# Kernel optimization log

Hardware: AMD Instinct MI355X
Metric: run time of the kernel (lower is better)

The kernel has to match this reference:

```python
import jax, jax.numpy as jnp
import numpy as np

B, T, C = 256, 1024, 128


def setup_inputs() -> dict:
    key = jax.random.key(0)
    k1, k2 = jax.random.split(key)
    potentials = jax.random.normal(k1, (B, T, C), dtype=jnp.float32)
    # glorot_uniform init for the [C, C] transition matrix
    limit = float(np.sqrt(6.0 / (C + C)))
    transitions = jax.random.uniform(k2, (C, C), minval=-limit, maxval=limit, dtype=jnp.float32)
    return {"potentials": potentials, "transitions": transitions}


def _viterbi_decode(potentials, transitions):
    """Equivalent of tfa.text.crf.crf_decode with full sequence lengths ('reg' mode).

    potentials: [B, T, C] unary scores; transitions: [C, C] (prev -> cur).
    Returns one-hot decoded tags [B, T, C] (the layer's inference output).
    """
    num_tags = potentials.shape[-1]
    pots_t = jnp.swapaxes(potentials, 0, 1)  # [T, B, C]
    alpha0 = pots_t[0]                        # [B, C]

    def fwd_step(alpha, pot):
        # max-plus DP step: scores[b, p, c] = alpha[b, p] + transitions[p, c]
        scores = alpha[:, :, None] + transitions[None, :, :]   # [B, C, C]
        bp = jnp.argmax(scores, axis=1).astype(jnp.int32)      # backpointers [B, C]
        alpha_new = jnp.max(scores, axis=1) + pot               # [B, C]
        return alpha_new, bp

    alpha_T, bps = jax.lax.scan(fwd_step, alpha0, pots_t[1:])   # bps: [T-1, B, C]
    last_tag = jnp.argmax(alpha_T, axis=-1).astype(jnp.int32)   # [B]

    def bwd_step(tag, bp):
        # tag at time t+1 -> best tag at time t via backpointers
        prev = jnp.take_along_axis(bp, tag[:, None], axis=1)[:, 0]
        return prev, prev

    _, prev_tags = jax.lax.scan(bwd_step, last_tag, bps, reverse=True)  # [T-1, B]
    tags = jnp.concatenate([prev_tags, last_tag[None, :]], axis=0)      # [T, B]
    tags = jnp.swapaxes(tags, 0, 1)                                      # [B, T]
    return jax.nn.one_hot(tags, num_tags, dtype=potentials.dtype)


def reference(potentials, transitions):
    return _viterbi_decode(potentials, transitions)
```

## Files before the change

### kernel.cpp

```cpp
#include <hip/hip_runtime.h>


typedef float f32x2 __attribute__((ext_vector_type(2)));
typedef unsigned int u32x4 __attribute__((ext_vector_type(4)));

constexpr int NB = 256;
constexpr int NT = 1024;
constexpr int NC = 128;

template <int CTRL>
__device__ __forceinline__ float fmax_dpp(float v) {
  int x = __builtin_amdgcn_update_dpp(__float_as_int(v), __float_as_int(v),
                                      CTRL, 0xF, 0xF, false);
  return fmaxf(v, __int_as_float(x));
}
__device__ __forceinline__ float wave_max_to_lane63(float m) {
  m = fmax_dpp<0x111>(m);
  m = fmax_dpp<0x112>(m);
  m = fmax_dpp<0x114>(m);
  m = fmax_dpp<0x118>(m);
  m = fmax_dpp<0x142>(m);
  m = fmax_dpp<0x143>(m);
  return m;
}

constexpr int ABUF = 192;

#define T_C(T0, T1, T2, T3, MD)                              \
  "v_pk_add_f32 v[52:53], v[60:61], %[" T0 "]\n\t"           \
  "v_pk_add_f32 v[54:55], v[62:63], %[" T1 "]\n\t"           \
  "v_pk_add_f32 v[46:47], v[56:57], %[" T2 "]\n\t"           \
  "v_pk_add_f32 v[44:45], v[58:59], %[" T3 "]\n\t"           \
  "v_max3_f32 v52, v52, v53, v54\n\t"                        \
  "v_max3_f32 v55, v55, v46, v47\n\t"                        \
  "v_max3_f32 v52, v52, v55, v44\n\t"                        \
  "v_max_f32 " MD ", v52, v45\n\t"

#define DPP4(CTL)                                                          \
  "v_max_f32_dpp v48, v48, v48 " CTL " row_mask:0xf bank_mask:0xf\n\t"     \
  "v_max_f32_dpp v49, v49, v49 " CTL " row_mask:0xf bank_mask:0xf\n\t"     \
  "v_max_f32_dpp v50, v50, v50 " CTL " row_mask:0xf bank_mask:0xf\n\t"     \
  "v_max_f32_dpp v51, v51, v51 " CTL " row_mask:0xf bank_mask:0xf\n\t"

#define STEP_S(RD, WR, PC, SOFF)                                           \
  "ds_read_b128 v[60:63], %[" RD "]\n\t"                                   \
  "ds_read_b128 v[56:59], %[" RD "] offset:16\n\t"                         \
  "s_waitcnt lgkmcnt(0)\n\t"                                               \
  T_C("t00", "t01", "t02", "t03", "v48")                                   \
  T_C("t10", "t11", "t12", "t13", "v49")                                   \
  T_C("t20", "t21", "t22", "t23", "v50")                                   \
  T_C("t30", "t31", "t32", "t33", "v51")                                   \
  DPP4("quad_perm:[1,0,3,2]")                                              \
  DPP4("quad_perm:[2,3,0,1]")                                              \
  DPP4("row_ror:4")                                                        \
  DPP4("row_ror:8")                                                        \
  "v_cndmask_b32 v46, v48, v49, %[sel1]\n\t"                               \
  "v_cndmask_b32 v47, v50, v51, %[sel1]\n\t"                               \
  "v_cndmask_b32 v47, v46, v47, %[sel2]\n\t"                               \
  "s_mov_b64 exec, %[wmask]\n\t"                                           \
  "v_add_f32 v46, v47, %[" PC "]\n\t"                                      \
  "ds_write_b32 %[" WR "], v46\n\t"                                        \
  "global_store_dword %[qoff], v47, %[sout] offset:" SOFF "\n\t"           \
  "s_mov_b64 exec, -1\n\t"                                                 \
  "s_waitcnt lgkmcnt(0)\n\t"                                               \
  "s_barrier\n\t"

__global__ __launch_bounds__(512, 2)
void crf_fwd(const float* __restrict__ pot, const float* __restrict__ trans,
             float* __restrict__ out) {
  __shared__ __align__(16) float alpha[2 * ABUF];

  const int tid = threadIdx.x;
  const int b = blockIdx.x;
  const int w = tid >> 6;
  const int l = tid & 63;
  const int r = l >> 4;
  const int i = l & 15;
  const int g = w * 4 + r;
  const bool wr = (i >= 12);
  const int cw = 4 * g + (i & 3);
  const int widx = 12 * (cw >> 3) + (cw & 7);

  const float* potb = pot + (size_t)b * NT * NC;
  float* outb = out + (size_t)b * NT * NC;

  const float* tb = trans + (8 * i) * NC + 4 * g;
  float4 L0 = *(const float4*)(tb + 0 * NC);
  float4 L1 = *(const float4*)(tb + 1 * NC);
  float4 L2 = *(const float4*)(tb + 2 * NC);
  float4 L3 = *(const float4*)(tb + 3 * NC);
  float4 L4 = *(const float4*)(tb + 4 * NC);
  float4 L5 = *(const float4*)(tb + 5 * NC);
  float4 L6 = *(const float4*)(tb + 6 * NC);
  float4 L7 = *(const float4*)(tb + 7 * NC);
  f32x2 t00 = {L0.x, L1.x}, t01 = {L2.x, L3.x}, t02 = {L4.x, L5.x}, t03 = {L6.x, L7.x};
  f32x2 t10 = {L0.y, L1.y}, t11 = {L2.y, L3.y}, t12 = {L4.y, L5.y}, t13 = {L6.y, L7.y};
  f32x2 t20 = {L0.z, L1.z}, t21 = {L2.z, L3.z}, t22 = {L4.z, L5.z}, t23 = {L6.z, L7.z};
  f32x2 t30 = {L0.w, L1.w}, t31 = {L2.w, L3.w}, t32 = {L4.w, L5.w}, t33 = {L6.w, L7.w};

  unsigned rda = (unsigned)(size_t)(alpha + 12 * i);
  unsigned rdb = (unsigned)(size_t)(alpha + ABUF + 12 * i);
  unsigned wra = (unsigned)(size_t)(alpha + widx);
  unsigned wrb = (unsigned)(size_t)(alpha + ABUF + widx);

  unsigned qoff = (unsigned)((1 * NC + cw) * 4);
  unsigned poff = ((unsigned)b * (NT * NC) + 5 * NC + cw) * 4u;
  unsigned long long sout = (unsigned long long)(size_t)outb;
  unsigned long long pbase = (unsigned long long)(size_t)pot;
  u32x4 srd;
  srd.x = (unsigned)pbase;
  srd.y = (unsigned)(pbase >> 32) & 0xFFFFu;
  srd.z = (unsigned)(NB * NT * NC) * 4u;
  srd.w = 0x00020000u;
  unsigned long long sel1 = 0xAAAAAAAAAAAAAAAAull;
  unsigned long long sel2 = 0xCCCCCCCCCCCCCCCCull;
  unsigned long long wmask = 0xF000F000F000F000ull;
  int cnt = 254;

  float pc0 = potb[1 * NC + cw], pc1 = potb[2 * NC + cw];
  float pc2 = potb[3 * NC + cw], pc3 = potb[4 * NC + cw];
  float pn0 = 0.f, pn1 = 0.f, pn2 = 0.f, pn3 = 0.f;

  if (wr) {
    alpha[widx] = potb[cw];
    outb[cw] = 0.0f;
  }
  __syncthreads();

  asm volatile(
      "buffer_load_dword %[pn0], %[poff], %[srd], 0 offen\n\t"
      "buffer_load_dword %[pn1], %[poff], %[srd], 0 offen offset:512\n\t"
      "buffer_load_dword %[pn2], %[poff], %[srd], 0 offen offset:1024\n\t"
      "buffer_load_dword %[pn3], %[poff], %[srd], 0 offen offset:1536\n\t"
      "L_crfmain_%=:\n\t"
      STEP_S("rda", "wrb", "pc0", "0")
      STEP_S("rdb", "wra", "pc1", "512")
      STEP_S("rda", "wrb", "pc2", "1024")
      STEP_S("rdb", "wra", "pc3", "1536")
      "s_waitcnt vmcnt(4)\n\t"
      "v_mov_b32 %[pc0], %[pn0]\n\t"
      "v_mov_b32 %[pc1], %[pn1]\n\t"
      "v_mov_b32 %[pc2], %[pn2]\n\t"
      "v_mov_b32 %[pc3], %[pn3]\n\t"
      "v_add_u32 %[poff], 0x800, %[poff]\n\t"
      "v_add_u32 %[qoff], 0x800, %[qoff]\n\t"
      "buffer_load_dword %[pn0], %[poff], %[srd], 0 offen\n\t"
      "buffer_load_dword %[pn1], %[poff], %[srd], 0 offen offset:512\n\t"
      "buffer_load_dword %[pn2], %[poff], %[srd], 0 offen offset:1024\n\t"
      "buffer_load_dword %[pn3], %[poff], %[srd], 0 offen offset:1536\n\t"
      "s_sub_u32 %[cnt], %[cnt], 1\n\t"
      "s_cmp_lg_u32 %[cnt], 0\n\t"
      "s_cbranch_scc1 L_crfmain_%=\n\t"
      STEP_S("rda", "wrb", "pc0", "0")
      STEP_S("rdb", "wra", "pc1", "512")
      STEP_S("rda", "wrb", "pc2", "1024")
      STEP_S("rdb", "wra", "pc3", "1536")
      "s_waitcnt vmcnt(4)\n\t"
      "v_mov_b32 %[pc0], %[pn0]\n\t"
      "v_mov_b32 %[pc1], %[pn1]\n\t"
      "v_mov_b32 %[pc2], %[pn2]\n\t"
      "v_add_u32 %[qoff], 0x800, %[qoff]\n\t"
      STEP_S("rda", "wrb", "pc0", "0")
      STEP_S("rdb", "wra", "pc1", "512")
      STEP_S("rda", "wrb", "pc2", "1024")
      : [pc0] "+v"(pc0), [pc1] "+v"(pc1), [pc2] "+v"(pc2), [pc3] "+v"(pc3),
        [pn0] "+v"(pn0), [pn1] "+v"(pn1), [pn2] "+v"(pn2), [pn3] "+v"(pn3),
        [qoff] "+v"(qoff), [poff] "+v"(poff), [cnt] "+s"(cnt)
      : [t00] "v"(t00), [t01] "v"(t01), [t02] "v"(t02), [t03] "v"(t03),
        [t10] "v"(t10), [t11] "v"(t11), [t12] "v"(t12), [t13] "v"(t13),
        [t20] "v"(t20), [t21] "v"(t21), [t22] "v"(t22), [t23] "v"(t23),
        [t30] "v"(t30), [t31] "v"(t31), [t32] "v"(t32), [t33] "v"(t33),
        [rda] "v"(rda), [rdb] "v"(rdb), [wra] "v"(wra), [wrb] "v"(wrb),
        [sout] "s"(sout), [srd] "s"(srd),
        [sel1] "s"(sel1), [sel2] "s"(sel2), [wmask] "s"(wmask)
      : "memory", "scc",
        "v44", "v45", "v46", "v47", "v48", "v49", "v50", "v51",
        "v52", "v53", "v54", "v55", "v56", "v57", "v58", "v59",
        "v60", "v61", "v62", "v63");
}


__global__ __launch_bounds__(256)
void crf_bwd(const float* __restrict__ pot, const float* __restrict__ trans,
             float* __restrict__ out) {
  extern __shared__ float tTf[];
  const int tid = threadIdx.x;
  const int b = blockIdx.x;
  const float* potb = pot + (size_t)b * NT * NC;
  float* outb = out + (size_t)b * NT * NC;

  {
    const int rr = tid >> 1;
    const int h = tid & 1;
    const float4* src = (const float4*)(trans + rr * NC + h * 64);
    const int lo = rr & 63, hb = rr >> 6;
    #pragma unroll
    for (int j = 0; j < 16; ++j) {
      float4 q = src[j];
      int cb = h * 64 + 4 * j;
      tTf[(cb + 0) * 128 + lo * 2 + hb] = q.x;
      tTf[(cb + 1) * 128 + lo * 2 + hb] = q.y;
      tTf[(cb + 2) * 128 + lo * 2 + hb] = q.z;
      tTf[(cb + 3) * 128 + lo * 2 + hb] = q.w;
    }
  }
  __syncthreads();
  if (tid >= 64) return;
  const int l = tid;
  const f32x2* tTp = (const f32x2*)tTf;

  float qlo_t = outb[(NT - 1) * NC + l];
  float qhi_t = outb[(NT - 1) * NC + 64 + l];
  float alo_t = qlo_t + potb[(NT - 1) * NC + l];
  float ahi_t = qhi_t + potb[(NT - 1) * NC + 64 + l];
  float m0 = wave_max_to_lane63(fmaxf(alo_t, ahi_t));
  float M0 = __int_as_float(__builtin_amdgcn_readlane(__float_as_int(m0), 63));
  unsigned long long bl = __ballot(alo_t == M0);
  unsigned long long bh = __ballot(ahi_t == M0);
  int tag = bl ? (__ffsll((long long)bl) - 1)
               : (64 + __ffsll((long long)bh) - 1);

  float cqlo[8], cqhi[8], calo[8], cahi[8];
  float nqlo[8], nqhi[8], nplo[8], nphi[8];
  #pragma unroll
  for (int j = 0; j < 8; ++j) {
    int rw = NT - 2 - j;
    cqlo[j] = outb[rw * NC + l];
    cqhi[j] = outb[rw * NC + 64 + l];
    calo[j] = cqlo[j] + potb[rw * NC + l];
    cahi[j] = cqhi[j] + potb[rw * NC + 64 + l];
  }

  for (int g = 0; g < 128; ++g) {
    #pragma unroll
    for (int j = 0; j < 8; ++j) {
      int rw = NT - 10 - 8 * g - j;
      if (rw < 0) rw = 0;
      nqlo[j] = outb[rw * NC + l];
      nqhi[j] = outb[rw * NC + 64 + l];
      nplo[j] = potb[rw * NC + l];
      nphi[j] = potb[rw * NC + 64 + l];
    }
    #pragma unroll
    for (int j = 0; j < 8; ++j) {
      int t = NT - 1 - 8 * g - j;
      if (t >= 1) {
        outb[t * NC + l]      = (l == tag) ? 1.0f : 0.0f;
        outb[t * NC + 64 + l] = (64 + l == tag) ? 1.0f : 0.0f;
        int Mlo = __builtin_amdgcn_readlane(__float_as_int(qlo_t), tag & 63);
        int Mhi = __builtin_amdgcn_readlane(__float_as_int(qhi_t), tag & 63);
        float M = __int_as_float((tag < 64) ? Mlo : Mhi);
        f32x2 tt = tTp[tag * 64 + l];
        float vlo = calo[j] + tt.x;
        float vhi = cahi[j] + tt.y;
        unsigned long long el = __ballot(vlo == M);
        unsigned long long eh = __ballot(vhi == M);
        tag = el ? (__ffsll((long long)el) - 1)
                 : (64 + __ffsll((long long)eh) - 1);
        qlo_t = cqlo[j];
        qhi_t = cqhi[j];
      }
    }
    #pragma unroll
    for (int j = 0; j < 8; ++j) {
      cqlo[j] = nqlo[j]; cqhi[j] = nqhi[j];
      calo[j] = nqlo[j] + nplo[j];
      cahi[j] = nqhi[j] + nphi[j];
    }
  }
  outb[l]      = (l == tag) ? 1.0f : 0.0f;
  outb[64 + l] = (64 + l == tag) ? 1.0f : 0.0f;
}


extern "C" void kernel_launch(void* const* d_in, const int* in_sizes, int n_in,
                              void* d_out, int out_size, void* d_ws, size_t ws_size,
                              hipStream_t stream) {
  const float* pot   = (const float*)d_in[0];
  const float* trans = (const float*)d_in[1];
  float* out = (float*)d_out;

  hipFuncSetAttribute((const void*)crf_bwd,
                      hipFuncAttributeMaxDynamicSharedMemorySize, NC * NC * 4);

  crf_fwd<<<NB, 512, 0, stream>>>(pot, trans, out);
  crf_bwd<<<NB, 256, NC * NC * 4, stream>>>(pot, trans, out);
}
```

Baseline: 436.3 us.

## Fuse forward and backward Viterbi kernels with 256-thread blocks, 8 tags per group

Merges the forward max-plus scan and the backtrace into one kernel, removing the second launch. It also halves the forward block to 256 threads, with each group handling 8 tags instead of 4. The transition slice per lane now lives in 64 explicitly named VGPRs, loaded by inline global loads. This doubles per-lane ALU work per step but halves the number of waves that meet at each barrier, and it drops occupancy to one block per CU.

```diff
diff --git a/kernel.cpp b/kernel.cpp
--- a/kernel.cpp
+++ b/kernel.cpp
@@ -26,49 +26,74 @@
 
 constexpr int ABUF = 192;
 
-#define T_C(T0, T1, T2, T3, MD)                              \
-  "v_pk_add_f32 v[52:53], v[60:61], %[" T0 "]\n\t"           \
-  "v_pk_add_f32 v[54:55], v[62:63], %[" T1 "]\n\t"           \
-  "v_pk_add_f32 v[46:47], v[56:57], %[" T2 "]\n\t"           \
-  "v_pk_add_f32 v[44:45], v[58:59], %[" T3 "]\n\t"           \
-  "v_max3_f32 v52, v52, v53, v54\n\t"                        \
-  "v_max3_f32 v55, v55, v46, v47\n\t"                        \
-  "v_max3_f32 v52, v52, v55, v44\n\t"                        \
-  "v_max_f32 " MD ", v52, v45\n\t"
-
-#define DPP4(CTL)                                                          \
+
+#define LDT(R, O) "global_load_dword v" R ", %[toff], %[strans] offset:" O "\n\t"
+
+#define TREE2(A0, A2, A4, A6, MDA, B0, B2, B4, B6, MDB)     \
+  "v_pk_add_f32 v[32:33], v[56:57], v[" A0 "]\n\t"          \
+  "v_pk_add_f32 v[40:41], v[56:57], v[" B0 "]\n\t"          \
+  "v_pk_add_f32 v[34:35], v[58:59], v[" A2 "]\n\t"          \
+  "v_pk_add_f32 v[42:43], v[58:59], v[" B2 "]\n\t"          \
+  "v_pk_add_f32 v[36:37], v[60:61], v[" A4 "]\n\t"          \
+  "v_pk_add_f32 v[44:45], v[60:61], v[" B4 "]\n\t"          \
+  "v_pk_add_f32 v[38:39], v[62:63], v[" A6 "]\n\t"          \
+  "v_pk_add_f32 v[46:47], v[62:63], v[" B6 "]\n\t"          \
+  "v_max3_f32 v32, v32, v33, v34\n\t"                       \
+  "v_max3_f32 v40, v40, v41, v42\n\t"                       \
+  "v_max3_f32 v35, v35, v36, v37\n\t"                       \
+  "v_max3_f32 v43, v43, v44, v45\n\t"                       \
+  "v_max3_f32 v32, v32, v35, v38\n\t"                       \
+  "v_max3_f32 v40, v40, v43, v46\n\t"                       \
+  "v_max_f32 " MDA ", v32, v39\n\t"                         \
+  "v_max_f32 " MDB ", v40, v47\n\t"
+
+#define DPP8(CTL)                                                          \
   "v_max_f32_dpp v48, v48, v48 " CTL " row_mask:0xf bank_mask:0xf\n\t"     \
   "v_max_f32_dpp v49, v49, v49 " CTL " row_mask:0xf bank_mask:0xf\n\t"     \
   "v_max_f32_dpp v50, v50, v50 " CTL " row_mask:0xf bank_mask:0xf\n\t"     \
-  "v_max_f32_dpp v51, v51, v51 " CTL " row_mask:0xf bank_mask:0xf\n\t"
+  "v_max_f32_dpp v51, v51, v51 " CTL " row_mask:0xf bank_mask:0xf\n\t"     \
+  "v_max_f32_dpp v52, v52, v52 " CTL " row_mask:0xf bank_mask:0xf\n\t"     \
+  "v_max_f32_dpp v53, v53, v53 " CTL " row_mask:0xf bank_mask:0xf\n\t"     \
+  "v_max_f32_dpp v54, v54, v54 " CTL " row_mask:0xf bank_mask:0xf\n\t"     \
+  "v_max_f32_dpp v55, v55, v55 " CTL " row_mask:0xf bank_mask:0xf\n\t"
 
 #define STEP_S(RD, WR, PC, SOFF)                                           \
-  "ds_read_b128 v[60:63], %[" RD "]\n\t"                                   \
-  "ds_read_b128 v[56:59], %[" RD "] offset:16\n\t"                         \
+  "ds_read_b128 v[56:59], %[" RD "]\n\t"                                   \
+  "ds_read_b128 v[60:63], %[" RD "] offset:16\n\t"                         \
   "s_waitcnt lgkmcnt(0)\n\t"                                               \
-  T_C("t00", "t01", "t02", "t03", "v48")                                   \
-  T_C("t10", "t11", "t12", "t13", "v49")                                   \
-  T_C("t20", "t21", "t22", "t23", "v50")                                   \
-  T_C("t30", "t31", "t32", "t33", "v51")                                   \
-  DPP4("quad_perm:[1,0,3,2]")                                              \
-  DPP4("quad_perm:[2,3,0,1]")                                              \
-  DPP4("row_ror:4")                                                        \
-  DPP4("row_ror:8")                                                        \
-  "v_cndmask_b32 v46, v48, v49, %[sel1]\n\t"                               \
-  "v_cndmask_b32 v47, v50, v51, %[sel1]\n\t"                               \
-  "v_cndmask_b32 v47, v46, v47, %[sel2]\n\t"                               \
+  TREE2("64:65","66:67","68:69","70:71","v48",                             \
+        "72:73","74:75","76:77","78:79","v49")                             \
+  TREE2("80:81","82:83","84:85","86:87","v50",                             \
+        "88:89","90:91","92:93","94:95","v51")                             \
+  TREE2("96:97","98:99","100:101","102:103","v52",                         \
+        "104:105","106:107","108:109","110:111","v53")                     \
+  TREE2("112:113","114:115","116:117","118:119","v54",                     \
+        "120:121","122:123","124:125","126:127","v55")                     \
+  DPP8("quad_perm:[1,0,3,2]")                                              \
+  DPP8("quad_perm:[2,3,0,1]")                                              \
+  DPP8("row_ror:4")                                                        \
+  DPP8("row_ror:8")                                                        \
+  "v_cndmask_b32 v32, v48, v49, %[selb0]\n\t"                              \
+  "v_cndmask_b32 v33, v50, v51, %[selb0]\n\t"                              \
+  "v_cndmask_b32 v34, v52, v53, %[selb0]\n\t"                              \
+  "v_cndmask_b32 v35, v54, v55, %[selb0]\n\t"                              \
+  "v_cndmask_b32 v32, v32, v33, %[selb1]\n\t"                              \
+  "v_cndmask_b32 v34, v34, v35, %[selb1]\n\t"                              \
+  "v_cndmask_b32 v32, v32, v34, %[selb2]\n\t"                              \
   "s_mov_b64 exec, %[wmask]\n\t"                                           \
-  "v_add_f32 v46, v47, %[" PC "]\n\t"                                      \
-  "ds_write_b32 %[" WR "], v46\n\t"                                        \
-  "global_store_dword %[qoff], v47, %[sout] offset:" SOFF "\n\t"           \
+  "v_add_f32 v33, v32, %[" PC "]\n\t"                                      \
+  "ds_write_b32 %[" WR "], v33\n\t"                                        \
+  "global_store_dword %[qoff], v32, %[sout] offset:" SOFF "\n\t"           \
   "s_mov_b64 exec, -1\n\t"                                                 \
   "s_waitcnt lgkmcnt(0)\n\t"                                               \
   "s_barrier\n\t"
 
-__global__ __launch_bounds__(512, 2)
-void crf_fwd(const float* __restrict__ pot, const float* __restrict__ trans,
-             float* __restrict__ out) {
-  __shared__ __align__(16) float alpha[2 * ABUF];
+__global__ __launch_bounds__(256, 1)
+void crf_fused(const float* __restrict__ pot, const float* __restrict__ trans,
+               float* __restrict__ out) {
+  extern __shared__ __align__(16) float smem[];
+  float* alpha = smem;
+  float* tTf = smem + 2 * ABUF;
 
   const int tid = threadIdx.x;
   const int b = blockIdx.x;
@@ -76,35 +101,23 @@
   const int l = tid & 63;
   const int r = l >> 4;
   const int i = l & 15;
-  const int g = w * 4 + r;
-  const bool wr = (i >= 12);
-  const int cw = 4 * g + (i & 3);
-  const int widx = 12 * (cw >> 3) + (cw & 7);
+  const int G = w * 4 + r;
+  const bool wr = (i >= 8);
+  const int cw = 8 * G + (i & 7);
+  const int widx = 12 * G + (i & 7);
 
   const float* potb = pot + (size_t)b * NT * NC;
   float* outb = out + (size_t)b * NT * NC;
-
-  const float* tb = trans + (8 * i) * NC + 4 * g;
-  float4 L0 = *(const float4*)(tb + 0 * NC);
-  float4 L1 = *(const float4*)(tb + 1 * NC);
-  float4 L2 = *(const float4*)(tb + 2 * NC);
-  float4 L3 = *(const float4*)(tb + 3 * NC);
-  float4 L4 = *(const float4*)(tb + 4 * NC);
-  float4 L5 = *(const float4*)(tb + 5 * NC);
-  float4 L6 = *(const float4*)(tb + 6 * NC);
-  float4 L7 = *(const float4*)(tb + 7 * NC);
-  f32x2 t00 = {L0.x, L1.x}, t01 = {L2.x, L3.x}, t02 = {L4.x, L5.x}, t03 = {L6.x, L7.x};
-  f32x2 t10 = {L0.y, L1.y}, t11 = {L2.y, L3.y}, t12 = {L4.y, L5.y}, t13 = {L6.y, L7.y};
-  f32x2 t20 = {L0.z, L1.z}, t21 = {L2.z, L3.z}, t22 = {L4.z, L5.z}, t23 = {L6.z, L7.z};
-  f32x2 t30 = {L0.w, L1.w}, t31 = {L2.w, L3.w}, t32 = {L4.w, L5.w}, t33 = {L6.w, L7.w};
 
   unsigned rda = (unsigned)(size_t)(alpha + 12 * i);
   unsigned rdb = (unsigned)(size_t)(alpha + ABUF + 12 * i);
   unsigned wra = (unsigned)(size_t)(alpha + widx);
   unsigned wrb = (unsigned)(size_t)(alpha + ABUF + widx);
 
+  unsigned toff = (unsigned)((8 * i * NC + 8 * G) * 4);
   unsigned qoff = (unsigned)((1 * NC + cw) * 4);
   unsigned poff = ((unsigned)b * (NT * NC) + 5 * NC + cw) * 4u;
+  unsigned long long strans = (unsigned long long)(size_t)trans;
   unsigned long long sout = (unsigned long long)(size_t)outb;
   unsigned long long pbase = (unsigned long long)(size_t)pot;
   u32x4 srd;
@@ -112,9 +125,10 @@
   srd.y = (unsigned)(pbase >> 32) & 0xFFFFu;
   srd.z = (unsigned)(NB * NT * NC) * 4u;
   srd.w = 0x00020000u;
-  unsigned long long sel1 = 0xAAAAAAAAAAAAAAAAull;
-  unsigned long long sel2 = 0xCCCCCCCCCCCCCCCCull;
-  unsigned long long wmask = 0xF000F000F000F000ull;
+  unsigned long long selb0 = 0xAAAAAAAAAAAAAAAAull;
+  unsigned long long selb1 = 0xCCCCCCCCCCCCCCCCull;
+  unsigned long long selb2 = 0xF0F0F0F0F0F0F0F0ull;
+  unsigned long long wmask = 0xFF00FF00FF00FF00ull;
   int cnt = 254;
 
   float pc0 = potb[1 * NC + cw], pc1 = potb[2 * NC + cw];
@@ -128,6 +142,23 @@
   __syncthreads();
 
   asm volatile(
+      LDT("64","0")   LDT("72","4")   LDT("80","8")   LDT("88","12")
+      LDT("96","16")  LDT("104","20") LDT("112","24") LDT("120","28")
+      LDT("65","512") LDT("73","516") LDT("81","520") LDT("89","524")
+      LDT("97","528") LDT("105","532") LDT("113","536") LDT("121","540")
+      LDT("66","1024") LDT("74","1028") LDT("82","1032") LDT("90","1036")
+      LDT("98","1040") LDT("106","1044") LDT("114","1048") LDT("122","1052")
+      LDT("67","1536") LDT("75","1540") LDT("83","1544") LDT("91","1548")
+      LDT("99","1552") LDT("107","1556") LDT("115","1560") LDT("123","1564")
+      LDT("68","2048") LDT("76","2052") LDT("84","2056") LDT("92","2060")
+      LDT("100","2064") LDT("108","2068") LDT("116","2072") LDT("124","2076")
+      LDT("69","2560") LDT("77","2564") LDT("85","2568") LDT("93","2572")
+      LDT("101","2576") LDT("109","2580") LDT("117","2584") LDT("125","2588")
+      LDT("70","3072") LDT("78","3076") LDT("86","3080") LDT("94","3084")
+      LDT("102","3088") LDT("110","3092") LDT("118","3096") LDT("126","3100")
+      LDT("71","3584") LDT("79","3588") LDT("87","3592") LDT("95","3596")
+      LDT("103","3600") LDT("111","3604") LDT("119","3608") LDT("127","3612")
+      "s_waitcnt vmcnt(0)\n\t"
       "buffer_load_dword %[pn0], %[poff], %[srd], 0 offen\n\t"
       "buffer_load_dword %[pn1], %[poff], %[srd], 0 offen offset:512\n\t"
       "buffer_load_dword %[pn2], %[poff], %[srd], 0 offen offset:1024\n\t"
@@ -163,32 +194,30 @@
       STEP_S("rda", "wrb", "pc0", "0")
       STEP_S("rdb", "wra", "pc1", "512")
       STEP_S("rda", "wrb", "pc2", "1024")
+      "s_waitcnt vmcnt(0)\n\t"
       : [pc0] "+v"(pc0), [pc1] "+v"(pc1), [pc2] "+v"(pc2), [pc3] "+v"(pc3),
         [pn0] "+v"(pn0), [pn1] "+v"(pn1), [pn2] "+v"(pn2), [pn3] "+v"(pn3),
         [qoff] "+v"(qoff), [poff] "+v"(poff), [cnt] "+s"(cnt)
-      : [t00] "v"(t00), [t01] "v"(t01), [t02] "v"(t02), [t03] "v"(t03),
-        [t10] "v"(t10), [t11] "v"(t11), [t12] "v"(t12), [t13] "v"(t13),
-        [t20] "v"(t20), [t21] "v"(t21), [t22] "v"(t22), [t23] "v"(t23),
-        [t30] "v"(t30), [t31] "v"(t31), [t32] "v"(t32), [t33] "v"(t33),
-        [rda] "v"(rda), [rdb] "v"(rdb), [wra] "v"(wra), [wrb] "v"(wrb),
-        [sout] "s"(sout), [srd] "s"(srd),
-        [sel1] "s"(sel1), [sel2] "s"(sel2), [wmask] "s"(wmask)
+      : [toff] "v"(toff), [rda] "v"(rda), [rdb] "v"(rdb),
+        [wra] "v"(wra), [wrb] "v"(wrb),
+        [strans] "s"(strans), [sout] "s"(sout), [srd] "s"(srd),
+        [selb0] "s"(selb0), [selb1] "s"(selb1), [selb2] "s"(selb2),
+        [wmask] "s"(wmask)
       : "memory", "scc",
-        "v44", "v45", "v46", "v47", "v48", "v49", "v50", "v51",
-        "v52", "v53", "v54", "v55", "v56", "v57", "v58", "v59",
-        "v60", "v61", "v62", "v63");
-}
-
-
-__global__ __launch_bounds__(256)
-void crf_bwd(const float* __restrict__ pot, const float* __restrict__ trans,
-             float* __restrict__ out) {
-  extern __shared__ float tTf[];
-  const int tid = threadIdx.x;
-  const int b = blockIdx.x;
-  const float* potb = pot + (size_t)b * NT * NC;
-  float* outb = out + (size_t)b * NT * NC;
-
+        "v32", "v33", "v34", "v35", "v36", "v37", "v38", "v39",
+        "v40", "v41", "v42", "v43", "v44", "v45", "v46", "v47",
+        "v48", "v49", "v50", "v51", "v52", "v53", "v54", "v55",
+        "v56", "v57", "v58", "v59", "v60", "v61", "v62", "v63",
+        "v64", "v65", "v66", "v67", "v68", "v69", "v70", "v71",
+        "v72", "v73", "v74", "v75", "v76", "v77", "v78", "v79",
+        "v80", "v81", "v82", "v83", "v84", "v85", "v86", "v87",
+        "v88", "v89", "v90", "v91", "v92", "v93", "v94", "v95",
+        "v96", "v97", "v98", "v99", "v100", "v101", "v102", "v103",
+        "v104", "v105", "v106", "v107", "v108", "v109", "v110", "v111",
+        "v112", "v113", "v114", "v115", "v116", "v117", "v118", "v119",
+        "v120", "v121", "v122", "v123", "v124", "v125", "v126", "v127");
+
+  __syncthreads();
   {
     const int rr = tid >> 1;
     const int h = tid & 1;
@@ -206,7 +235,6 @@
   }
   __syncthreads();
   if (tid >= 64) return;
-  const int l = tid;
   const f32x2* tTp = (const f32x2*)tTf;
 
   float qlo_t = outb[(NT - 1) * NC + l];
@@ -280,9 +308,9 @@
   const float* trans = (const float*)d_in[1];
   float* out = (float*)d_out;
 
-  hipFuncSetAttribute((const void*)crf_bwd,
-                      hipFuncAttributeMaxDynamicSharedMemorySize, NC * NC * 4);
-
-  crf_fwd<<<NB, 512, 0, stream>>>(pot, trans, out);
-  crf_bwd<<<NB, 256, NC * NC * 4, stream>>>(pot, trans, out);
+  constexpr int SMEM = (2 * ABUF + NC * NC) * 4;
+  hipFuncSetAttribute((const void*)crf_fused,
+                      hipFuncAttributeMaxDynamicSharedMemorySize, SMEM);
+
+  crf_fused<<<NB, 256, SMEM, stream>>>(pot, trans, out);
 }
```

Measured after the change: 443.2 us. About the same (+1.6%).

## Remap forward Viterbi threads to 16 predecessors by 2 tags per lane

Applied to the files above, without the earlier changes.

The forward max-plus kernel changes its work split. Each lane now reduces 16 predecessors for 2 current tags, instead of 8 predecessors for 4 tags. The cross-lane DPP reduction drops from four shuffle rounds over four values to three rounds over two values, and the select chain gets shorter. Transition values now load directly into hard-coded registers inside the asm, and LDS reads per step double. This cuts per-step serial latency but raises register pressure and clobbers many VGPRs, which could limit occupancy at 2 blocks per CU.

```diff
diff --git a/kernel.cpp b/kernel.cpp
--- a/kernel.cpp
+++ b/kernel.cpp
@@ -26,44 +26,71 @@
 
 constexpr int ABUF = 192;
 
-#define T_C(T0, T1, T2, T3, MD)                              \
-  "v_pk_add_f32 v[52:53], v[60:61], %[" T0 "]\n\t"           \
-  "v_pk_add_f32 v[54:55], v[62:63], %[" T1 "]\n\t"           \
-  "v_pk_add_f32 v[46:47], v[56:57], %[" T2 "]\n\t"           \
-  "v_pk_add_f32 v[44:45], v[58:59], %[" T3 "]\n\t"           \
-  "v_max3_f32 v52, v52, v53, v54\n\t"                        \
-  "v_max3_f32 v55, v55, v46, v47\n\t"                        \
-  "v_max3_f32 v52, v52, v55, v44\n\t"                        \
-  "v_max_f32 " MD ", v52, v45\n\t"
-
-#define DPP4(CTL)                                                          \
-  "v_max_f32_dpp v48, v48, v48 " CTL " row_mask:0xf bank_mask:0xf\n\t"     \
-  "v_max_f32_dpp v49, v49, v49 " CTL " row_mask:0xf bank_mask:0xf\n\t"     \
-  "v_max_f32_dpp v50, v50, v50 " CTL " row_mask:0xf bank_mask:0xf\n\t"     \
-  "v_max_f32_dpp v51, v51, v51 " CTL " row_mask:0xf bank_mask:0xf\n\t"
+#define TREEA                                             \
+  "v_pk_add_f32 v[32:33], v[48:49], v[64:65]\n\t"         \
+  "v_pk_add_f32 v[34:35], v[50:51], v[66:67]\n\t"         \
+  "v_pk_add_f32 v[36:37], v[52:53], v[68:69]\n\t"         \
+  "v_pk_add_f32 v[38:39], v[54:55], v[70:71]\n\t"         \
+  "v_pk_add_f32 v[40:41], v[56:57], v[72:73]\n\t"         \
+  "v_pk_add_f32 v[42:43], v[58:59], v[74:75]\n\t"         \
+  "v_pk_add_f32 v[44:45], v[60:61], v[76:77]\n\t"         \
+  "v_pk_add_f32 v[46:47], v[62:63], v[78:79]\n\t"         \
+  "v_max3_f32 v32, v32, v33, v34\n\t"                     \
+  "v_max3_f32 v35, v35, v36, v37\n\t"                     \
+  "v_max3_f32 v38, v38, v39, v40\n\t"                     \
+  "v_max3_f32 v41, v41, v42, v43\n\t"                     \
+  "v_max3_f32 v44, v44, v45, v46\n\t"                     \
+  "v_max3_f32 v32, v32, v35, v38\n\t"                     \
+  "v_max3_f32 v41, v41, v44, v47\n\t"                     \
+  "v_max_f32 v32, v32, v41\n\t"
+
+#define TREEB                                             \
+  "v_pk_add_f32 v[96:97], v[48:49], v[80:81]\n\t"         \
+  "v_pk_add_f32 v[98:99], v[50:51], v[82:83]\n\t"         \
+  "v_pk_add_f32 v[100:101], v[52:53], v[84:85]\n\t"       \
+  "v_pk_add_f32 v[102:103], v[54:55], v[86:87]\n\t"       \
+  "v_pk_add_f32 v[104:105], v[56:57], v[88:89]\n\t"       \
+  "v_pk_add_f32 v[106:107], v[58:59], v[90:91]\n\t"       \
+  "v_pk_add_f32 v[108:109], v[60:61], v[92:93]\n\t"       \
+  "v_pk_add_f32 v[110:111], v[62:63], v[94:95]\n\t"       \
+  "v_max3_f32 v96, v96, v97, v98\n\t"                     \
+  "v_max3_f32 v99, v99, v100, v101\n\t"                   \
+  "v_max3_f32 v102, v102, v103, v104\n\t"                 \
+  "v_max3_f32 v105, v105, v106, v107\n\t"                 \
+  "v_max3_f32 v108, v108, v109, v110\n\t"                 \
+  "v_max3_f32 v96, v96, v99, v102\n\t"                    \
+  "v_max3_f32 v105, v105, v108, v111\n\t"                 \
+  "v_max_f32 v96, v96, v105\n\t"
+
+#define DPP2(CTL)                                                          \
+  "v_max_f32_dpp v32, v32, v32 " CTL " row_mask:0xf bank_mask:0xf\n\t"     \
+  "v_max_f32_dpp v96, v96, v96 " CTL " row_mask:0xf bank_mask:0xf\n\t"
 
 #define STEP_S(RD, WR, PC, SOFF)                                           \
-  "ds_read_b128 v[60:63], %[" RD "]\n\t"                                   \
-  "ds_read_b128 v[56:59], %[" RD "] offset:16\n\t"                         \
+  "ds_read_b128 v[48:51], %[" RD "]\n\t"                                   \
+  "ds_read_b128 v[52:55], %[" RD "] offset:16\n\t"                         \
+  "ds_read_b128 v[56:59], %[" RD "] offset:48\n\t"                         \
+  "ds_read_b128 v[60:63], %[" RD "] offset:64\n\t"                         \
   "s_waitcnt lgkmcnt(0)\n\t"                                               \
-  T_C("t00", "t01", "t02", "t03", "v48")                                   \
-  T_C("t10", "t11", "t12", "t13", "v49")                                   \
-  T_C("t20", "t21", "t22", "t23", "v50")                                   \
-  T_C("t30", "t31", "t32", "t33", "v51")                                   \
-  DPP4("quad_perm:[1,0,3,2]")                                              \
-  DPP4("quad_perm:[2,3,0,1]")                                              \
-  DPP4("row_ror:4")                                                        \
-  DPP4("row_ror:8")                                                        \
-  "v_cndmask_b32 v46, v48, v49, %[sel1]\n\t"                               \
-  "v_cndmask_b32 v47, v50, v51, %[sel1]\n\t"                               \
-  "v_cndmask_b32 v47, v46, v47, %[sel2]\n\t"                               \
+  TREEA                                                                    \
+  TREEB                                                                    \
+  "s_nop 1\n\t"                                                            \
+  DPP2("quad_perm:[1,0,3,2]")                                              \
+  "s_nop 0\n\t"                                                            \
+  DPP2("quad_perm:[2,3,0,1]")                                              \
+  "s_nop 0\n\t"                                                            \
+  DPP2("row_half_mirror")                                                  \
+  "s_nop 0\n\t"                                                            \
+  "v_cndmask_b32 v41, v32, v96, %[selb0]\n\t"                              \
   "s_mov_b64 exec, %[wmask]\n\t"                                           \
-  "v_add_f32 v46, v47, %[" PC "]\n\t"                                      \
-  "ds_write_b32 %[" WR "], v46\n\t"                                        \
-  "global_store_dword %[qoff], v47, %[sout] offset:" SOFF "\n\t"           \
+  "v_add_f32 v40, v41, %[" PC "]\n\t"                                      \
+  "ds_write_b32 %[" WR "], v40\n\t"                                        \
+  "global_store_dword %[qoff], v41, %[sout] offset:" SOFF "\n\t"           \
   "s_mov_b64 exec, -1\n\t"                                                 \
   "s_waitcnt lgkmcnt(0)\n\t"                                               \
   "s_barrier\n\t"
+
+#define LDT(R, B, O) "global_load_dword v" R ", %[" B "], %[strans] offset:" O "\n\t"
 
 __global__ __launch_bounds__(512, 2)
 void crf_fwd(const float* __restrict__ pot, const float* __restrict__ trans,
@@ -74,37 +101,26 @@
   const int b = blockIdx.x;
   const int w = tid >> 6;
   const int l = tid & 63;
-  const int r = l >> 4;
-  const int i = l & 15;
-  const int g = w * 4 + r;
-  const bool wr = (i >= 12);
-  const int cw = 4 * g + (i & 3);
+  const int g = l >> 3;
+  const int i = l & 7;
+  const int G = w * 8 + g;
+  const bool wr = (l & 7) < 2;
+  const int cw = 16 * w + 2 * g + (l & 1);
   const int widx = 12 * (cw >> 3) + (cw & 7);
 
   const float* potb = pot + (size_t)b * NT * NC;
   float* outb = out + (size_t)b * NT * NC;
 
-  const float* tb = trans + (8 * i) * NC + 4 * g;
-  float4 L0 = *(const float4*)(tb + 0 * NC);
-  float4 L1 = *(const float4*)(tb + 1 * NC);
-  float4 L2 = *(const float4*)(tb + 2 * NC);
-  float4 L3 = *(const float4*)(tb + 3 * NC);
-  float4 L4 = *(const float4*)(tb + 4 * NC);
-  float4 L5 = *(const float4*)(tb + 5 * NC);
-  float4 L6 = *(const float4*)(tb + 6 * NC);
-  float4 L7 = *(const float4*)(tb + 7 * NC);
-  f32x2 t00 = {L0.x, L1.x}, t01 = {L2.x, L3.x}, t02 = {L4.x, L5.x}, t03 = {L6.x, L7.x};
-  f32x2 t10 = {L0.y, L1.y}, t11 = {L2.y, L3.y}, t12 = {L4.y, L5.y}, t13 = {L6.y, L7.y};
-  f32x2 t20 = {L0.z, L1.z}, t21 = {L2.z, L3.z}, t22 = {L4.z, L5.z}, t23 = {L6.z, L7.z};
-  f32x2 t30 = {L0.w, L1.w}, t31 = {L2.w, L3.w}, t32 = {L4.w, L5.w}, t33 = {L6.w, L7.w};
-
-  unsigned rda = (unsigned)(size_t)(alpha + 12 * i);
-  unsigned rdb = (unsigned)(size_t)(alpha + ABUF + 12 * i);
+  unsigned rda = (unsigned)(size_t)(alpha + 24 * i);
+  unsigned rdb = (unsigned)(size_t)(alpha + ABUF + 24 * i);
   unsigned wra = (unsigned)(size_t)(alpha + widx);
   unsigned wrb = (unsigned)(size_t)(alpha + ABUF + widx);
 
+  unsigned toff  = (unsigned)((16 * i * NC + 2 * G) * 4);
+  unsigned toff2 = toff + 4096;
   unsigned qoff = (unsigned)((1 * NC + cw) * 4);
   unsigned poff = ((unsigned)b * (NT * NC) + 5 * NC + cw) * 4u;
+  unsigned long long strans = (unsigned long long)(size_t)trans;
   unsigned long long sout = (unsigned long long)(size_t)outb;
   unsigned long long pbase = (unsigned long long)(size_t)pot;
   u32x4 srd;
@@ -112,9 +128,8 @@
   srd.y = (unsigned)(pbase >> 32) & 0xFFFFu;
   srd.z = (unsigned)(NB * NT * NC) * 4u;
   srd.w = 0x00020000u;
-  unsigned long long sel1 = 0xAAAAAAAAAAAAAAAAull;
-  unsigned long long sel2 = 0xCCCCCCCCCCCCCCCCull;
-  unsigned long long wmask = 0xF000F000F000F000ull;
+  unsigned long long selb0 = 0xAAAAAAAAAAAAAAAAull;
+  unsigned long long wmask = 0x0303030303030303ull;
   int cnt = 254;
 
   float pc0 = potb[1 * NC + cw], pc1 = potb[2 * NC + cw];
@@ -128,6 +143,23 @@
   __syncthreads();
 
   asm volatile(
+      LDT("64","toff","0")     LDT("65","toff","512")
+      LDT("66","toff","1024")  LDT("67","toff","1536")
+      LDT("68","toff","2048")  LDT("69","toff","2560")
+      LDT("70","toff","3072")  LDT("71","toff","3584")
+      LDT("72","toff2","0")    LDT("73","toff2","512")
+      LDT("74","toff2","1024") LDT("75","toff2","1536")
+      LDT("76","toff2","2048") LDT("77","toff2","2560")
+      LDT("78","toff2","3072") LDT("79","toff2","3584")
+      LDT("80","toff","4")     LDT("81","toff","516")
+      LDT("82","toff","1028")  LDT("83","toff","1540")
+      LDT("84","toff","2052")  LDT("85","toff","2564")
+      LDT("86","toff","3076")  LDT("87","toff","3588")
+      LDT("88","toff2","4")    LDT("89","toff2","516")
+      LDT("90","toff2","1028") LDT("91","toff2","1540")
+      LDT("92","toff2","2052") LDT("93","toff2","2564")
+      LDT("94","toff2","3076") LDT("95","toff2","3588")
+      "s_waitcnt vmcnt(0)\n\t"
       "buffer_load_dword %[pn0], %[poff], %[srd], 0 offen\n\t"
       "buffer_load_dword %[pn1], %[poff], %[srd], 0 offen offset:512\n\t"
       "buffer_load_dword %[pn2], %[poff], %[srd], 0 offen offset:1024\n\t"
@@ -166,17 +198,21 @@
       : [pc0] "+v"(pc0), [pc1] "+v"(pc1), [pc2] "+v"(pc2), [pc3] "+v"(pc3),
         [pn0] "+v"(pn0), [pn1] "+v"(pn1), [pn2] "+v"(pn2), [pn3] "+v"(pn3),
         [qoff] "+v"(qoff), [poff] "+v"(poff), [cnt] "+s"(cnt)
-      : [t00] "v"(t00), [t01] "v"(t01), [t02] "v"(t02), [t03] "v"(t03),
-        [t10] "v"(t10), [t11] "v"(t11), [t12] "v"(t12), [t13] "v"(t13),
-        [t20] "v"(t20), [t21] "v"(t21), [t22] "v"(t22), [t23] "v"(t23),
-        [t30] "v"(t30), [t31] "v"(t31), [t32] "v"(t32), [t33] "v"(t33),
+      : [toff] "v"(toff), [toff2] "v"(toff2),
         [rda] "v"(rda), [rdb] "v"(rdb), [wra] "v"(wra), [wrb] "v"(wrb),
-        [sout] "s"(sout), [srd] "s"(srd),
-        [sel1] "s"(sel1), [sel2] "s"(sel2), [wmask] "s"(wmask)
+        [strans] "s"(strans), [sout] "s"(sout), [srd] "s"(srd),
+        [selb0] "s"(selb0), [wmask] "s"(wmask)
       : "memory", "scc",
-        "v44", "v45", "v46", "v47", "v48", "v49", "v50", "v51",
-        "v52", "v53", "v54", "v55", "v56", "v57", "v58", "v59",
-        "v60", "v61", "v62", "v63");
+        "v32", "v33", "v34", "v35", "v36", "v37", "v38", "v39",
+        "v40", "v41", "v42", "v43", "v44", "v45", "v46", "v47",
+        "v48", "v49", "v50", "v51", "v52", "v53", "v54", "v55",
+        "v56", "v57", "v58", "v59", "v60", "v61", "v62", "v63",
+        "v64", "v65", "v66", "v67", "v68", "v69", "v70", "v71",
+        "v72", "v73", "v74", "v75", "v76", "v77", "v78", "v79",
+        "v80", "v81", "v82", "v83", "v84", "v85", "v86", "v87",
+        "v88", "v89", "v90", "v91", "v92", "v93", "v94", "v95",
+        "v96", "v97", "v98", "v99", "v100", "v101", "v102", "v103",
+        "v104", "v105", "v106", "v107", "v108", "v109", "v110", "v111");
 }
 
 
```

After: 418.9 us. -4.0%, faster.
